# Performance work log

Hardware: AMD Instinct MI355X
Metric: run time of the kernel (lower is better)

Reference implementation:

```python
import jax, jax.numpy as jnp
import numpy as np

V, D, S, B = 32000, 1024, 2048, 4
H = 4 * D


def _sinusoidal_pe(max_len, d):
    position = np.arange(max_len, dtype=np.float32)[:, None]
    div_term = np.exp(np.arange(0, d, 2, dtype=np.float32) * (-np.log(10000.0) / d))
    pe = np.zeros((max_len, d), dtype=np.float32)
    pe[:, 0::2] = np.sin(position * div_term)
    pe[:, 1::2] = np.cos(position * div_term)
    return jnp.asarray(pe)


def setup_inputs() -> dict:
    key = jax.random.key(0)
    ks = jax.random.split(key, 13)
    std = 1.0 / np.sqrt(D)
    stdh = 1.0 / np.sqrt(H)
    w = lambda k, shp, s: (jax.random.normal(k, shp, jnp.float32) * s)
    inp = {
        "tokens": jax.random.randint(ks[0], (B, S), 0, V),
        "emb": jax.random.normal(ks[1], (V, D), jnp.float32),
        "pe": _sinusoidal_pe(S, D),
        "l1_wk": w(ks[2], (D, D), std),
        "l1_wv": w(ks[3], (D, D), std),
        "l1_wo": w(ks[4], (D, D), std),
        "l1_w1": w(ks[5], (D, H), std),
        "l1_w2": w(ks[6], (H, D), stdh),
        "l2_wk": w(ks[7], (D, D), std),
        "l2_wv": w(ks[8], (D, D), std),
        "l2_wo": w(ks[9], (D, D), std),
        "l2_w1": w(ks[10], (D, H), std),
        "l2_w2": w(ks[11], (H, D), stdh),
        "w_out": w(ks[12], (D, V), std),
    }
    return inp


def _block(h, mask, wk, wv, wo, w1, w2):
    d = h.shape[-1]
    xq = h                      # W_q is identity
    xk = h @ wk                 # [B,S,D]
    xv = h @ wv
    scores = jnp.einsum("bsd,btd->bst", xq, xk) / np.sqrt(float(d)) + mask
    attn = jax.nn.softmax(scores, axis=-1)          # [B,S,S]
    h_attn = jnp.einsum("bst,btd->bsd", attn, xv) @ wo
    h_res = h + h_attn
    h_ffn = jnp.maximum(h_res @ w1, 0.0) @ w2
    return h_res + h_ffn


def reference(tokens, emb, pe, l1_wk, l1_wv, l1_wo, l1_w1, l1_w2,
              l2_wk, l2_wv, l2_wo, l2_w1, l2_w2, w_out):
    seq_len = tokens.shape[1]
    h = emb[tokens] + pe[None, :seq_len, :]
    # causal additive mask: -inf above diagonal
    mask = jnp.triu(jnp.full((seq_len, seq_len), -jnp.inf, jnp.float32), k=1)
    h = _block(h, mask, l1_wk, l1_wv, l1_wo, l1_w1, l1_w2)
    h = _block(h, mask, l2_wk, l2_wv, l2_wo, l2_w1, l2_w2)
    logits = h[:, -1, :] @ w_out  # [B, V]
    return logits
```

## Files before the change

kernel.cpp:

```cpp
#include <hip/hip_runtime.h>

#define S_LEN 2048
#define D_DIM 1024
#define H_DIM 4096
#define V_DIM 32000
#define B_SZ  4

typedef float  f32x4  __attribute__((ext_vector_type(4)));
typedef __bf16 bf16x8 __attribute__((ext_vector_type(8)));

__device__ __forceinline__ ushort f2bf(float f) {
    union { float f; unsigned u; } v; v.f = f;
    unsigned r = v.u + 0x7fffu + ((v.u >> 16) & 1u);
    return (ushort)(r >> 16);
}

__global__ void bt_wtranspose(const float* __restrict__ in, ushort* __restrict__ out,
                              int R, int C) {
    __shared__ ushort s[64][65];
    int r0 = blockIdx.y * 64, c0 = blockIdx.x * 64;
    int t = threadIdx.x;
    int lr = t >> 2, lc4 = (t & 3) * 16;
    const float* src = in + (size_t)(r0 + lr) * C + c0 + lc4;
#pragma unroll
    for (int j = 0; j < 4; ++j) {
        float4 v = ((const float4*)src)[j];
        s[lr][lc4 + 4 * j + 0] = f2bf(v.x);
        s[lr][lc4 + 4 * j + 1] = f2bf(v.y);
        s[lr][lc4 + 4 * j + 2] = f2bf(v.z);
        s[lr][lc4 + 4 * j + 3] = f2bf(v.w);
    }
    __syncthreads();
    int oc = t >> 2, orr = (t & 3) * 16;
    ushort tmp[16] __attribute__((aligned(16)));
#pragma unroll
    for (int j = 0; j < 16; ++j) tmp[j] = s[orr + j][oc];
    ushort* dst = out + (size_t)(c0 + oc) * R + r0 + orr;
    *(uint4*)dst        = *(uint4*)tmp;
    *(uint4*)(dst + 8)  = *(uint4*)(tmp + 8);
}

__global__ void bt_transpose(const ushort* __restrict__ in, ushort* __restrict__ out,
                             int R, int C) {
    __shared__ ushort s[64][65];
    int r0 = blockIdx.y * 64, c0 = blockIdx.x * 64;
    int t = threadIdx.x;
    int lr = t >> 2, lc = (t & 3) * 16;
    const ushort* src = in + (size_t)(r0 + lr) * C + c0 + lc;
    uint4 v0 = ((const uint4*)src)[0];
    uint4 v1 = ((const uint4*)src)[1];
    ushort tin[16] __attribute__((aligned(16)));
    *(uint4*)tin = v0; *(uint4*)(tin + 8) = v1;
#pragma unroll
    for (int j = 0; j < 16; ++j) s[lr][lc + j] = tin[j];
    __syncthreads();
    int oc = t >> 2, orr = (t & 3) * 16;
    ushort tmp[16] __attribute__((aligned(16)));
#pragma unroll
    for (int j = 0; j < 16; ++j) tmp[j] = s[orr + j][oc];
    ushort* dst = out + (size_t)(c0 + oc) * R + r0 + orr;
    *(uint4*)dst       = *(uint4*)tmp;
    *(uint4*)(dst + 8) = *(uint4*)(tmp + 8);
}

__global__ void bt_embed(const int* __restrict__ tokens, const float* __restrict__ emb,
                         const float* __restrict__ pe, float* __restrict__ h,
                         ushort* __restrict__ hbf) {
    int row = blockIdx.x;
    int s   = row & (S_LEN - 1);
    int tok = tokens[row];
    int t   = threadIdx.x;
    float4 v = ((const float4*)(emb + (size_t)tok * D_DIM))[t];
    float4 p = ((const float4*)(pe + (size_t)s * D_DIM))[t];
    v.x += p.x; v.y += p.y; v.z += p.z; v.w += p.w;
    ((float4*)(h + (size_t)row * D_DIM))[t] = v;
    uint2 pk;
    pk.x = (unsigned)f2bf(v.x) | ((unsigned)f2bf(v.y) << 16);
    pk.y = (unsigned)f2bf(v.z) | ((unsigned)f2bf(v.w) << 16);
    ((uint2*)(hbf + (size_t)row * D_DIM))[t] = pk;
}

#define EPI_F32  0
#define EPI_BF16 1
#define EPI_RELU 2
#define EPI_RES  3

#define VMWAIT(N) asm volatile("s_waitcnt vmcnt(%0)" :: "n"(N) : "memory")
#define SBAR()    __builtin_amdgcn_s_barrier()
#define MEMPIN()  asm volatile("" ::: "memory")
#define AS1 __attribute__((address_space(1)))
#define AS3 __attribute__((address_space(3)))

template <int BM, int BN, int NW, int WCc, int EPI, bool CSKIP, bool KLIM, int SWZ>
__global__ __launch_bounds__(NW * 64, (NW == 8 ? 2 : 1))
void bt_gemm(const ushort* __restrict__ A, const ushort* __restrict__ B,
             float* Cf, ushort* Cb, const float* __restrict__ Res,
             int lda, int ldb, int ldc, int K,
             size_t strideA, size_t strideB, size_t strideC) {
    constexpr int WRr = NW / WCc;
    constexpr int MR  = BM / (16 * WRr);
    constexpr int NR  = BN / (16 * WCc);
    constexpr int Ak  = BM / (16 * NW);
    constexpr int Bk  = BN / (16 * NW);
    constexpr int G   = Ak + Bk;
    constexpr int HS  = (BM + BN) * 32;

    __shared__ ushort lds[4][HS];

    int bm, bn;
    if (SWZ == 1) {
        int gx = gridDim.x, gy = gridDim.y;
        int id = blockIdx.y * gx + blockIdx.x;
        int xcd = id & 7, slot = id >> 3;
        int bandH = gy >> 3;
        bm = xcd * bandH + (slot % bandH);
        bn = slot / bandH;
    } else if (SWZ == 2) {
        int gx = gridDim.x;
        int id = blockIdx.y * gx + blockIdx.x;
        int xcd = id & 7, slot = id >> 3;
        int bandW = gx >> 3;
        bn = xcd * bandW + (slot % bandW);
        bm = slot / bandW;
    } else { bm = blockIdx.y; bn = blockIdx.x; }

    if (CSKIP && bn * BN >= (bm + 1) * BM) return;

    const int tid  = threadIdx.x;
    const int lane = tid & 63;
    const int wid  = tid >> 6;
    const int wr   = wid / WCc, wc = wid % WCc;
    const int r15  = lane & 15, r4 = lane >> 4;
    const int lr   = lane >> 2;
    const int lsl  = lane & 3;
    const int kswz = (r4 ^ ((r15 >> 1) & 3)) * 8;

    const ushort* Ab = A + strideA * blockIdx.z + (size_t)bm * BM * lda;
    const ushort* Bb = B + strideB * blockIdx.z + (size_t)bn * BN * ldb;

    int NT = K >> 6;
    if (KLIM) { int lim = (bm + 1) * (BM / 64); if (lim < NT) NT = lim; }
    const int NH2 = 2 * NT;

    f32x4 acc[MR][NR];
#pragma unroll
    for (int m = 0; m < MR; ++m)
#pragma unroll
        for (int n = 0; n < NR; ++n) acc[m][n] = (f32x4){0.f, 0.f, 0.f, 0.f};

    bf16x8 aqA[MR], aqB[MR], bq[NR];

#define STAGE(hs)                                                                 \
    {                                                                             \
        const int t_ = (hs) >> 1, b_ = (hs) & 3;                                  \
        const int c_ = ((hs) & 1) * 4 + (lsl ^ ((lr >> 1) & 3));                  \
        _Pragma("unroll")                                                         \
        for (int j = 0; j < Ak; ++j) {                                            \
            int row = (wid + j * NW) * 16 + lr;                                   \
            __builtin_amdgcn_global_load_lds(                                     \
                (const AS1 void*)(Ab + (size_t)t_ * 64 + (size_t)row * lda + c_ * 8), \
                (AS3 void*)(&lds[b_][0] + (wid + j * NW) * 512), 16, 0, 0);       \
        }                                                                         \
        _Pragma("unroll")                                                         \
        for (int j = 0; j < Bk; ++j) {                                            \
            int row = (wid + j * NW) * 16 + lr;                                   \
            __builtin_amdgcn_global_load_lds(                                     \
                (const AS1 void*)(Bb + (size_t)t_ * 64 + (size_t)row * ldb + c_ * 8), \
                (AS3 void*)(&lds[b_][BM * 32] + (wid + j * NW) * 512), 16, 0, 0); \
        }                                                                         \
    }

#define READ_A(hs, dst)                                                           \
    {                                                                             \
        const int b_ = (hs) & 3;                                                  \
        _Pragma("unroll")                                                         \
        for (int m = 0; m < MR; ++m) {                                            \
            int row = wr * (16 * MR) + m * 16 + r15;                              \
            dst[m] = *(const bf16x8*)(&lds[b_][row * 32 + kswz]);                 \
        }                                                                         \
    }

#define READ_B(hs)                                                                \
    {                                                                             \
        const int b_ = (hs) & 3;                                                  \
        _Pragma("unroll")                                                         \
        for (int n = 0; n < NR; ++n) {                                            \
            int col = wc * (16 * NR) + n * 16 + r15;                              \
            bq[n] = *(const bf16x8*)(&lds[b_][BM * 32 + col * 32 + kswz]);        \
        }                                                                         \
    }

#define CLUSTER(aset)                                                             \
    __builtin_amdgcn_s_setprio(1);                                                \
    _Pragma("unroll")                                                             \
    for (int m = 0; m < MR; ++m)                                                  \
        _Pragma("unroll")                                                         \
        for (int n = 0; n < NR; ++n)                                              \
            acc[m][n] = __builtin_amdgcn_mfma_f32_16x16x32_bf16(aset[m], bq[n], acc[m][n], 0, 0, 0); \
    __builtin_amdgcn_s_setprio(0);

    STAGE(0); STAGE(1);
    VMWAIT(G); SBAR(); MEMPIN();
    STAGE(2);
    READ_A(0, aqA);

    for (int t = 0; t < NT - 1; ++t) {
        const int hs = 2 * t;
        VMWAIT(G); SBAR(); MEMPIN();
        STAGE(hs + 3);
        READ_B(hs);
        READ_A(hs + 1, aqB);
        CLUSTER(aqA);
        VMWAIT(G); SBAR(); MEMPIN();
        if (t < NT - 2) STAGE(hs + 4);
        READ_B(hs + 1);
        READ_A(hs + 2, aqA);
        CLUSTER(aqB);
    }
    VMWAIT(0); SBAR(); MEMPIN();
    READ_B(NH2 - 2);
    READ_A(NH2 - 1, aqB);
    CLUSTER(aqA);
    READ_B(NH2 - 1);
    CLUSTER(aqB);

    size_t cz = strideC * blockIdx.z;
    const int rowb = bm * BM + wr * (16 * MR) + r4 * 4;
    const int colb = bn * BN + wc * (16 * NR) + r15;
#pragma unroll
    for (int m = 0; m < MR; ++m) {
#pragma unroll
        for (int r = 0; r < 4; ++r) {
            int row = rowb + m * 16 + r;
            size_t base = cz + (size_t)row * ldc + colb;
#pragma unroll
            for (int n = 0; n < NR; ++n) {
                float v = acc[m][n][r];
                size_t idx = base + n * 16;
                if (EPI == EPI_F32)       Cf[idx] = v;
                else if (EPI == EPI_BF16) Cb[idx] = f2bf(v);
                else if (EPI == EPI_RELU) Cb[idx] = f2bf(fmaxf(v, 0.f));
                else { float o = v + Res[idx]; Cf[idx] = o; Cb[idx] = f2bf(o); }
            }
        }
    }
#undef STAGE
#undef READ_A
#undef READ_B
#undef CLUSTER
}

__device__ __forceinline__ float wred_max(float v) {
#pragma unroll
    for (int off = 32; off; off >>= 1) v = fmaxf(v, __shfl_xor(v, off));
    return v;
}
__device__ __forceinline__ float wred_sum(float v) {
#pragma unroll
    for (int off = 32; off; off >>= 1) v += __shfl_xor(v, off);
    return v;
}

__global__ void bt_softmax(const float* __restrict__ scores, ushort* __restrict__ probs) {
    int row = blockIdx.x;
    int s   = row & (S_LEN - 1);
    const float* src = scores + (size_t)row * S_LEN;
    ushort*      dst = probs  + (size_t)row * S_LEN;
    int tid = threadIdx.x;
    int nvalid = s + 1;

    float vals[8];
    float mx = -1e30f;
#pragma unroll
    for (int j = 0; j < 8; ++j) {
        int t = tid + j * 256;
        float v = (t < nvalid) ? src[t] * 0.03125f : -1e30f;
        vals[j] = v;
        mx = fmaxf(mx, v);
    }
    __shared__ float red[4], red2[4];
    mx = wred_max(mx);
    if ((tid & 63) == 0) red[tid >> 6] = mx;
    __syncthreads();
    mx = fmaxf(fmaxf(red[0], red[1]), fmaxf(red[2], red[3]));

    float sum = 0.f, ps[8];
#pragma unroll
    for (int j = 0; j < 8; ++j) {
        float p = exp2f((vals[j] - mx) * 1.44269504f);
        ps[j] = p; sum += p;
    }
    sum = wred_sum(sum);
    if ((tid & 63) == 0) red2[tid >> 6] = sum;
    __syncthreads();
    sum = red2[0] + red2[1] + red2[2] + red2[3];
    float inv = 1.0f / sum;
#pragma unroll
    for (int j = 0; j < 8; ++j) {
        int t = tid + j * 256;
        dst[t] = (t < nvalid) ? f2bf(ps[j] * inv) : (ushort)0;
    }
}

__global__ void bt_logits(const float* __restrict__ h, const float* __restrict__ wout,
                          float* __restrict__ out) {
    __shared__ float hl[4][128];
    int tid = threadIdx.x;
    int d0 = blockIdx.y * 128;
    if (tid < 128) {
#pragma unroll
        for (int b = 0; b < 4; ++b)
            hl[b][tid] = h[((size_t)b * S_LEN + (S_LEN - 1)) * D_DIM + d0 + tid];
    }
    __syncthreads();
    int v = blockIdx.x * 256 + tid;
    float a0 = 0, a1 = 0, a2 = 0, a3 = 0;
    for (int j = 0; j < 128; ++j) {
        float w = wout[(size_t)(d0 + j) * V_DIM + v];
        a0 += hl[0][j] * w; a1 += hl[1][j] * w;
        a2 += hl[2][j] * w; a3 += hl[3][j] * w;
    }
    atomicAdd(out + v, a0);
    atomicAdd(out + V_DIM + v, a1);
    atomicAdd(out + 2 * V_DIM + v, a2);
    atomicAdd(out + 3 * V_DIM + v, a3);
}

extern "C" void kernel_launch(void* const* d_in, const int* in_sizes, int n_in,
                              void* d_out, int out_size, void* d_ws, size_t ws_size,
                              hipStream_t stream) {
    const int*   tokens = (const int*)d_in[0];
    const float* emb    = (const float*)d_in[1];
    const float* pe     = (const float*)d_in[2];
    const float* wgt[10];
    for (int i = 0; i < 10; ++i) wgt[i] = (const float*)d_in[3 + i];
    const float* wout = (const float*)d_in[13];

    char* w = (char*)d_ws;
    size_t o = 0;
    auto take = [&](size_t sz) { char* p = w + o; o += (sz + 255) & ~(size_t)255; return p; };

    const size_t DD = (size_t)D_DIM * D_DIM * 2;
    const size_t DH = (size_t)D_DIM * H_DIM * 2;
    size_t wsz[10] = {DD, DD, DD, DH, DH, DD, DD, DD, DH, DH};
    ushort* wT[10];
    for (int i = 0; i < 10; ++i) wT[i] = (ushort*)take(wsz[i]);

    const size_t NROW = (size_t)B_SZ * S_LEN;
    float*  h0     = (float*)take(NROW * D_DIM * 4);
    float*  h1     = (float*)take(NROW * D_DIM * 4);
    ushort* hbf    = (ushort*)take(NROW * D_DIM * 2);
    ushort* hresbf = (ushort*)take(NROW * D_DIM * 2);
    ushort* xkbf   = (ushort*)take(NROW * D_DIM * 2);
    ushort* xvt    = (ushort*)take((size_t)D_DIM * NROW * 2);
    ushort* hattn  = (ushort*)take(NROW * D_DIM * 2);
    char*   G      = take((size_t)B_SZ * S_LEN * S_LEN * 4 + (size_t)B_SZ * S_LEN * S_LEN * 2);
    float*  scores = (float*)G;
    ushort* probs  = (ushort*)(G + (size_t)B_SZ * S_LEN * S_LEN * 4);
    ushort* tbf    = (ushort*)G;

    int wR[10] = {1024, 1024, 1024, 1024, 4096, 1024, 1024, 1024, 1024, 4096};
    int wC[10] = {1024, 1024, 1024, 4096, 1024, 1024, 1024, 1024, 4096, 1024};
    for (int i = 0; i < 10; ++i)
        bt_wtranspose<<<dim3(wC[i] / 64, wR[i] / 64), 256, 0, stream>>>(wgt[i], wT[i], wR[i], wC[i]);

    bt_embed<<<NROW, 256, 0, stream>>>(tokens, emb, pe, h0, hbf);

    auto layer = [&](ushort* wk, ushort* wv2, ushort* wo, ushort* w1, ushort* w2) {
        bt_gemm<256, 128, 4, 2, EPI_BF16, false, false, 1><<<dim3(8, 32), 256, 0, stream>>>(
            hbf, wk, nullptr, xkbf, nullptr, D_DIM, D_DIM, D_DIM, D_DIM, 0, 0, 0);
        bt_gemm<256, 128, 4, 2, EPI_BF16, false, false, 1><<<dim3(8, 32), 256, 0, stream>>>(
            hbf, wv2, nullptr, hresbf, nullptr, D_DIM, D_DIM, D_DIM, D_DIM, 0, 0, 0);
        bt_transpose<<<dim3(D_DIM / 64, NROW / 64), 256, 0, stream>>>(
            hresbf, xvt, (int)NROW, D_DIM);
        bt_gemm<256, 128, 4, 2, EPI_F32, true, false, 0><<<dim3(16, 8, B_SZ), 256, 0, stream>>>(
            hbf, xkbf, scores, nullptr, nullptr, D_DIM, D_DIM, S_LEN, D_DIM,
            (size_t)S_LEN * D_DIM, (size_t)S_LEN * D_DIM, (size_t)S_LEN * S_LEN);
        bt_softmax<<<NROW, 256, 0, stream>>>(scores, probs);
        bt_gemm<256, 128, 4, 2, EPI_BF16, false, true, 0><<<dim3(8, 8, B_SZ), 256, 0, stream>>>(
            probs, xvt, nullptr, hattn, nullptr, S_LEN, (int)NROW, D_DIM, S_LEN,
            (size_t)S_LEN * S_LEN, (size_t)S_LEN, (size_t)S_LEN * D_DIM);
        bt_gemm<256, 128, 4, 2, EPI_RES, false, false, 1><<<dim3(8, 32), 256, 0, stream>>>(
            hattn, wo, h1, hresbf, h0, D_DIM, D_DIM, D_DIM, D_DIM, 0, 0, 0);
        bt_gemm<256, 256, 8, 4, EPI_RELU, false, false, 1><<<dim3(16, 32), 512, 0, stream>>>(
            hresbf, w1, nullptr, tbf, nullptr, D_DIM, D_DIM, H_DIM, D_DIM, 0, 0, 0);
        bt_gemm<256, 128, 4, 2, EPI_RES, false, false, 1><<<dim3(8, 32), 256, 0, stream>>>(
            tbf, w2, h0, hbf, h1, H_DIM, H_DIM, D_DIM, H_DIM, 0, 0, 0);
    };
    layer(wT[0], wT[1], wT[2], wT[3], wT[4]);
    layer(wT[5], wT[6], wT[7], wT[8], wT[9]);

    hipMemsetAsync(d_out, 0, (size_t)B_SZ * V_DIM * sizeof(float), stream);
    bt_logits<<<dim3(V_DIM / 256, D_DIM / 128), 256, 0, stream>>>(h0, wout, (float*)d_out);
}
```

Measured before the change: 988.5 us.

## Restructure GEMM mainloop into half-tile phases and shrink tiles to 128x128

The GEMM main loop is rewritten to stage 32-wide K slices in per-wave parts and to split each slice's MFMA work into two M-half phases. Each phase interleaves LDS reads, async global-to-LDS staging and barriers, with an explicit lgkmcnt wait and a sched_barrier. Most launches move from 256x128 to 128x128 tiles with twice as many blocks, and launch bounds change to allow two blocks per CU for 4-wave kernels. The intent is better latency hiding and occupancy, at the cost of more barriers per K step and lower per-block data reuse.

```diff
diff --git a/kernel.cpp b/kernel.cpp
--- a/kernel.cpp
+++ b/kernel.cpp
@@ -86,13 +86,14 @@
 #define EPI_RES  3
 
 #define VMWAIT(N) asm volatile("s_waitcnt vmcnt(%0)" :: "n"(N) : "memory")
+#define LGKM0()   asm volatile("s_waitcnt lgkmcnt(0)" ::: "memory")
 #define SBAR()    __builtin_amdgcn_s_barrier()
-#define MEMPIN()  asm volatile("" ::: "memory")
+#define SCHED0()  __builtin_amdgcn_sched_barrier(0)
 #define AS1 __attribute__((address_space(1)))
 #define AS3 __attribute__((address_space(3)))
 
 template <int BM, int BN, int NW, int WCc, int EPI, bool CSKIP, bool KLIM, int SWZ>
-__global__ __launch_bounds__(NW * 64, (NW == 8 ? 2 : 1))
+__global__ __launch_bounds__(NW * 64, (NW == 8 ? 1 : 2))
 void bt_gemm(const ushort* __restrict__ A, const ushort* __restrict__ B,
              float* Cf, ushort* Cb, const float* __restrict__ Res,
              int lda, int ldb, int ldc, int K,
@@ -100,12 +101,10 @@
     constexpr int WRr = NW / WCc;
     constexpr int MR  = BM / (16 * WRr);
     constexpr int NR  = BN / (16 * WCc);
-    constexpr int Ak  = BM / (16 * NW);
-    constexpr int Bk  = BN / (16 * NW);
-    constexpr int G   = Ak + Bk;
-    constexpr int HS  = (BM + BN) * 32;
-
-    __shared__ ushort lds[4][HS];
+    constexpr int MH  = MR / 2;
+    constexpr int SLOT = (BM + BN) * 32;
+
+    __shared__ ushort lds[4][SLOT];
 
     int bm, bn;
     if (SWZ == 1) {
@@ -148,81 +147,65 @@
 #pragma unroll
         for (int n = 0; n < NR; ++n) acc[m][n] = (f32x4){0.f, 0.f, 0.f, 0.f};
 
-    bf16x8 aqA[MR], aqB[MR], bq[NR];
-
-#define STAGE(hs)                                                                 \
+#define STAGE_PART(s_, p_)                                                        \
     {                                                                             \
-        const int t_ = (hs) >> 1, b_ = (hs) & 3;                                  \
-        const int c_ = ((hs) & 1) * 4 + (lsl ^ ((lr >> 1) & 3));                  \
+        const int b_ = (s_) & 3;                                                  \
+        const int c_ = lsl ^ ((lr >> 1) & 3);                                     \
+        const int rw_ = (wid + (p_) * NW) * 16 + lr;                              \
+        __builtin_amdgcn_global_load_lds(                                         \
+            (const AS1 void*)(Ab + (size_t)(s_) * 32 + (size_t)rw_ * lda + c_ * 8), \
+            (AS3 void*)(&lds[b_][0] + (wid + (p_) * NW) * 512), 16, 0, 0);        \
+        __builtin_amdgcn_global_load_lds(                                         \
+            (const AS1 void*)(Bb + (size_t)(s_) * 32 + (size_t)rw_ * ldb + c_ * 8), \
+            (AS3 void*)(&lds[b_][BM * 32] + (wid + (p_) * NW) * 512), 16, 0, 0);  \
+    }
+
+#define PHASE(s_, mh_, DOSTAGE)                                                   \
+    {                                                                             \
+        const int b_ = (s_) & 3;                                                  \
+        bf16x8 aq[MH], bq[NR];                                                    \
         _Pragma("unroll")                                                         \
-        for (int j = 0; j < Ak; ++j) {                                            \
-            int row = (wid + j * NW) * 16 + lr;                                   \
-            __builtin_amdgcn_global_load_lds(                                     \
-                (const AS1 void*)(Ab + (size_t)t_ * 64 + (size_t)row * lda + c_ * 8), \
-                (AS3 void*)(&lds[b_][0] + (wid + j * NW) * 512), 16, 0, 0);       \
+        for (int mm = 0; mm < MH; ++mm) {                                         \
+            int row = wr * (16 * MR) + ((mh_) * MH + mm) * 16 + r15;              \
+            aq[mm] = *(const bf16x8*)(&lds[b_][row * 32 + kswz]);                 \
         }                                                                         \
-        _Pragma("unroll")                                                         \
-        for (int j = 0; j < Bk; ++j) {                                            \
-            int row = (wid + j * NW) * 16 + lr;                                   \
-            __builtin_amdgcn_global_load_lds(                                     \
-                (const AS1 void*)(Bb + (size_t)t_ * 64 + (size_t)row * ldb + c_ * 8), \
-                (AS3 void*)(&lds[b_][BM * 32] + (wid + j * NW) * 512), 16, 0, 0); \
-        }                                                                         \
-    }
-
-#define READ_A(hs, dst)                                                           \
-    {                                                                             \
-        const int b_ = (hs) & 3;                                                  \
-        _Pragma("unroll")                                                         \
-        for (int m = 0; m < MR; ++m) {                                            \
-            int row = wr * (16 * MR) + m * 16 + r15;                              \
-            dst[m] = *(const bf16x8*)(&lds[b_][row * 32 + kswz]);                 \
-        }                                                                         \
-    }
-
-#define READ_B(hs)                                                                \
-    {                                                                             \
-        const int b_ = (hs) & 3;                                                  \
         _Pragma("unroll")                                                         \
         for (int n = 0; n < NR; ++n) {                                            \
             int col = wc * (16 * NR) + n * 16 + r15;                              \
             bq[n] = *(const bf16x8*)(&lds[b_][BM * 32 + col * 32 + kswz]);        \
         }                                                                         \
-    }
-
-#define CLUSTER(aset)                                                             \
-    __builtin_amdgcn_s_setprio(1);                                                \
-    _Pragma("unroll")                                                             \
-    for (int m = 0; m < MR; ++m)                                                  \
+        if (DOSTAGE) STAGE_PART((s_) + 3, mh_);                                   \
+        SBAR();                                                                   \
+        LGKM0(); SCHED0();                                                        \
+        __builtin_amdgcn_s_setprio(1);                                            \
         _Pragma("unroll")                                                         \
-        for (int n = 0; n < NR; ++n)                                              \
-            acc[m][n] = __builtin_amdgcn_mfma_f32_16x16x32_bf16(aset[m], bq[n], acc[m][n], 0, 0, 0); \
-    __builtin_amdgcn_s_setprio(0);
-
-    STAGE(0); STAGE(1);
-    VMWAIT(G); SBAR(); MEMPIN();
-    STAGE(2);
-    READ_A(0, aqA);
-
-    for (int t = 0; t < NT - 1; ++t) {
-        const int hs = 2 * t;
-        VMWAIT(G); SBAR(); MEMPIN();
-        STAGE(hs + 3);
-        READ_B(hs);
-        READ_A(hs + 1, aqB);
-        CLUSTER(aqA);
-        VMWAIT(G); SBAR(); MEMPIN();
-        if (t < NT - 2) STAGE(hs + 4);
-        READ_B(hs + 1);
-        READ_A(hs + 2, aqA);
-        CLUSTER(aqB);
-    }
-    VMWAIT(0); SBAR(); MEMPIN();
-    READ_B(NH2 - 2);
-    READ_A(NH2 - 1, aqB);
-    CLUSTER(aqA);
-    READ_B(NH2 - 1);
-    CLUSTER(aqB);
+        for (int mm = 0; mm < MH; ++mm)                                           \
+            _Pragma("unroll")                                                     \
+            for (int n = 0; n < NR; ++n)                                          \
+                acc[(mh_) * MH + mm][n] =                                         \
+                    __builtin_amdgcn_mfma_f32_16x16x32_bf16(aq[mm], bq[n],        \
+                        acc[(mh_) * MH + mm][n], 0, 0, 0);                        \
+        __builtin_amdgcn_s_setprio(0);                                            \
+    }
+
+    STAGE_PART(0, 0); STAGE_PART(0, 1);
+    STAGE_PART(1, 0); STAGE_PART(1, 1);
+    STAGE_PART(2, 0); STAGE_PART(2, 1);
+    VMWAIT(8); SBAR();
+
+    int s = 0;
+    for (; s < NH2 - 3; ++s) {
+        PHASE(s, 0, true);  SBAR();
+        PHASE(s, 1, true);  VMWAIT(8); SBAR();
+    }
+    PHASE(s, 0, false); SBAR();
+    PHASE(s, 1, false); VMWAIT(4); SBAR();
+    ++s;
+    PHASE(s, 0, false); SBAR();
+    PHASE(s, 1, false); VMWAIT(0); SBAR();
+    ++s;
+    PHASE(s, 0, false); SBAR();
+    PHASE(s, 1, false);
 
     size_t cz = strideC * blockIdx.z;
     const int rowb = bm * BM + wr * (16 * MR) + r4 * 4;
@@ -244,10 +227,8 @@
             }
         }
     }
-#undef STAGE
-#undef READ_A
-#undef READ_B
-#undef CLUSTER
+#undef STAGE_PART
+#undef PHASE
 }
 
 __device__ __forceinline__ float wred_max(float v) {
@@ -367,24 +348,24 @@
     bt_embed<<<NROW, 256, 0, stream>>>(tokens, emb, pe, h0, hbf);
 
     auto layer = [&](ushort* wk, ushort* wv2, ushort* wo, ushort* w1, ushort* w2) {
-        bt_gemm<256, 128, 4, 2, EPI_BF16, false, false, 1><<<dim3(8, 32), 256, 0, stream>>>(
+        bt_gemm<128, 128, 4, 2, EPI_BF16, false, false, 1><<<dim3(8, 64), 256, 0, stream>>>(
             hbf, wk, nullptr, xkbf, nullptr, D_DIM, D_DIM, D_DIM, D_DIM, 0, 0, 0);
-        bt_gemm<256, 128, 4, 2, EPI_BF16, false, false, 1><<<dim3(8, 32), 256, 0, stream>>>(
+        bt_gemm<128, 128, 4, 2, EPI_BF16, false, false, 1><<<dim3(8, 64), 256, 0, stream>>>(
             hbf, wv2, nullptr, hresbf, nullptr, D_DIM, D_DIM, D_DIM, D_DIM, 0, 0, 0);
         bt_transpose<<<dim3(D_DIM / 64, NROW / 64), 256, 0, stream>>>(
             hresbf, xvt, (int)NROW, D_DIM);
-        bt_gemm<256, 128, 4, 2, EPI_F32, true, false, 0><<<dim3(16, 8, B_SZ), 256, 0, stream>>>(
+        bt_gemm<128, 128, 4, 2, EPI_F32, true, false, 0><<<dim3(16, 16, B_SZ), 256, 0, stream>>>(
             hbf, xkbf, scores, nullptr, nullptr, D_DIM, D_DIM, S_LEN, D_DIM,
             (size_t)S_LEN * D_DIM, (size_t)S_LEN * D_DIM, (size_t)S_LEN * S_LEN);
         bt_softmax<<<NROW, 256, 0, stream>>>(scores, probs);
-        bt_gemm<256, 128, 4, 2, EPI_BF16, false, true, 0><<<dim3(8, 8, B_SZ), 256, 0, stream>>>(
+        bt_gemm<128, 128, 4, 2, EPI_BF16, false, true, 0><<<dim3(8, 16, B_SZ), 256, 0, stream>>>(
             probs, xvt, nullptr, hattn, nullptr, S_LEN, (int)NROW, D_DIM, S_LEN,
             (size_t)S_LEN * S_LEN, (size_t)S_LEN, (size_t)S_LEN * D_DIM);
-        bt_gemm<256, 128, 4, 2, EPI_RES, false, false, 1><<<dim3(8, 32), 256, 0, stream>>>(
+        bt_gemm<128, 128, 4, 2, EPI_RES, false, false, 1><<<dim3(8, 64), 256, 0, stream>>>(
             hattn, wo, h1, hresbf, h0, D_DIM, D_DIM, D_DIM, D_DIM, 0, 0, 0);
         bt_gemm<256, 256, 8, 4, EPI_RELU, false, false, 1><<<dim3(16, 32), 512, 0, stream>>>(
             hresbf, w1, nullptr, tbf, nullptr, D_DIM, D_DIM, H_DIM, D_DIM, 0, 0, 0);
-        bt_gemm<256, 128, 4, 2, EPI_RES, false, false, 1><<<dim3(8, 32), 256, 0, stream>>>(
+        bt_gemm<128, 128, 4, 2, EPI_RES, false, false, 1><<<dim3(8, 64), 256, 0, stream>>>(
             tbf, w2, h0, hbf, h1, H_DIM, H_DIM, D_DIM, H_DIM, 0, 0, 0);
     };
     layer(wT[0], wT[1], wT[2], wT[3], wT[4]);
```

Result: faster. 915.4 us (-7.4%).
